# Performance work log

Measured on AMD Instinct MI355X. Metric: run time of the kernel, lower is better.

The kernel has to match this reference:

```python
import jax, jax.numpy as jnp
import numpy as np

B, S, D = 8, 1024, 1024      # batch, seq_len, inp_dim
H, HD = 8, 64                # head_num, head_dim
HID = H * HD                 # hidden_dim = 512
P = 2 * D                    # p_factor * inp_dim = 2048
K = 4                        # causal conv kernel size
EPS = 1e-6
CAP = 15.0                   # soft cap for i/f gates


def _layernorm(x, g, b):
    mu = jnp.mean(x, -1, keepdims=True)
    var = jnp.var(x, -1, keepdims=True)
    return (x - mu) * jax.lax.rsqrt(var + EPS) * g + b


def _soft_cap(v):
    return CAP * jnp.tanh(v / CAP)


def _causal_conv_feat(x, w, b):
    # Conv1d(1,1,K) applied over the FEATURE axis of each timestep (as in the
    # torch code: x_t.unsqueeze(1) -> (bs,1,P)), causal left pad of K-1.
    L = x.shape[-1]
    xp = jnp.pad(x, ((0, 0), (0, 0), (K - 1, 0)))
    out = b
    for m in range(K):
        out = out + w[m] * xp[..., m:m + L]
    return out


def _forward(x, ln_g, ln_b, mh_g, mh_b, W_up_l, b_up_l, W_up_r, b_up_r,
             W_down, b_down, conv_w, conv_b, W_skip, b_skip, W_i, b_i,
             W_f, b_f, W_o, b_o, W_q, b_q, W_k, b_k, W_v, b_v):
    Bs, Sl, _ = x.shape
    xn = _layernorm(x, ln_g, ln_b)
    x_t = xn @ W_up_l.T + b_up_l                      # (B,S,P)
    r_t = xn @ W_up_r.T + b_up_r                      # (B,S,HID)
    x_c = jax.nn.silu(_causal_conv_feat(x_t, conv_w, conv_b))
    x_skip = x_c @ W_skip.T + b_skip                  # (B,S,HID)
    q = (x_c @ W_q.T + b_q).reshape(Bs, Sl, H, HD)
    k = (x_c @ W_k.T + b_k).reshape(Bs, Sl, H, HD) / float(np.sqrt(HD))
    v = (x_t @ W_v.T + b_v).reshape(Bs, Sl, H, HD)
    i_pre = _soft_cap(x_c @ W_i.T + b_i)              # (B,S,H)
    f_pre = _soft_cap(x_c @ W_f.T + b_f)              # (B,S,H)
    o = jax.nn.sigmoid(x_t @ W_o.T + b_o)             # (B,S,HID)

    def step(carry, inp):
        c, n, m = carry
        qt, kt, vt, it, ft = inp
        m_t = jnp.maximum(ft + m, it)
        ie = jnp.exp(it - m_t)
        fe = jnp.exp(ft - m_t + m)
        c = fe[:, :, None, None] * c + ie[:, :, None, None] * jnp.einsum('bhd,bhe->bhde', vt, kt)
        n = fe[:, :, None] * n + ie[:, :, None] * kt
        num = jnp.einsum('bhde,bhe->bhd', c, qt)
        den = jnp.maximum(jnp.sum(n * qt, -1, keepdims=True), 1.0)
        return (c, n, m_t), num / den

    c0 = jnp.zeros((Bs, H, HD, HD), x.dtype)
    n0 = jnp.ones((Bs, H, HD), x.dtype)
    m0 = jnp.zeros((Bs, H), x.dtype)
    seq = tuple(jnp.moveaxis(a, 1, 0) for a in (q, k, v, i_pre, f_pre))
    _, hs = jax.lax.scan(step, (c0, n0, m0), seq)     # hs: (S,B,H,HD)
    h = o * jnp.moveaxis(hs, 0, 1).reshape(Bs, Sl, HID)
    hn = _layernorm(h.reshape(Bs, Sl, H, HD), mh_g, mh_b).reshape(Bs, Sl, HID)
    out = (hn + x_skip) * jax.nn.silu(r_t)
    return out @ W_down.T + b_down + x


def setup_inputs() -> dict:
    key = jax.random.key(0)
    ks = jax.random.split(key, 16)

    def w(kk, shape):
        return jax.random.normal(kk, shape, jnp.float32) / np.sqrt(shape[-1]).astype(np.float32)

    return {
        'x': jax.random.normal(ks[0], (B, S, D), jnp.float32),
        'ln_g': jnp.ones((D,), jnp.float32), 'ln_b': jnp.zeros((D,), jnp.float32),
        'mh_g': jnp.ones((H, HD), jnp.float32), 'mh_b': jnp.zeros((H, HD), jnp.float32),
        'W_up_l': w(ks[1], (P, D)), 'b_up_l': jnp.zeros((P,), jnp.float32),
        'W_up_r': w(ks[2], (HID, D)), 'b_up_r': jnp.zeros((HID,), jnp.float32),
        'W_down': w(ks[3], (D, HID)), 'b_down': jnp.zeros((D,), jnp.float32),
        'conv_w': jax.random.normal(ks[4], (K,), jnp.float32) * 0.3,
        'conv_b': jnp.zeros((), jnp.float32),
        'W_skip': w(ks[5], (HID, P)), 'b_skip': jnp.zeros((HID,), jnp.float32),
        'W_i': w(ks[6], (H, P)), 'b_i': jnp.zeros((H,), jnp.float32),
        'W_f': w(ks[7], (H, P)), 'b_f': jnp.zeros((H,), jnp.float32),
        'W_o': w(ks[8], (HID, P)), 'b_o': jnp.zeros((HID,), jnp.float32),
        'W_q': w(ks[9], (HID, P)), 'b_q': jnp.zeros((HID,), jnp.float32),
        'W_k': w(ks[10], (HID, P)), 'b_k': jnp.zeros((HID,), jnp.float32),
        'W_v': w(ks[11], (HID, P)), 'b_v': jnp.zeros((HID,), jnp.float32),
    }


def reference(x, ln_g, ln_b, mh_g, mh_b, W_up_l, b_up_l, W_up_r, b_up_r,
              W_down, b_down, conv_w, conv_b, W_skip, b_skip, W_i, b_i,
              W_f, b_f, W_o, b_o, W_q, b_q, W_k, b_k, W_v, b_v):
    return _forward(x, ln_g, ln_b, mh_g, mh_b, W_up_l, b_up_l, W_up_r, b_up_r,
                    W_down, b_down, conv_w, conv_b, W_skip, b_skip, W_i, b_i,
                    W_f, b_f, W_o, b_o, W_q, b_q, W_k, b_k, W_v, b_v)
```

## Files before the change

kernel.cpp:

```cpp
#include <hip/hip_runtime.h>
#include <hip/hip_bf16.h>
#include <math.h>

#define Bq 8
#define Sq 1024
#define Dq 1024
#define Hq 8
#define HDq 64
#define HIDq 512
#define Pq 2048
#define EPSq 1e-6f
#define CAPq 15.0f
#define NCq 16
#define CLq 64
#define ARENA_SH 4096
#define BUF_SH   (4 * ARENA_SH)
#define GEMM_SMEM_BYTES (2 * BUF_SH * 2)

typedef __attribute__((ext_vector_type(8))) short short8;
typedef __attribute__((ext_vector_type(4))) float f32x4v;
typedef __hip_bfloat16 bf16;

__device__ inline void split2(float v, bf16& h, bf16& l) {
  h = __float2bfloat16(v);
  l = __float2bfloat16(v - __bfloat162float(h));
}

__device__ inline float bfs2f(short s) {
  bf16 t = *(const bf16*)&s;
  return __bfloat162float(t);
}

__global__ __launch_bounds__(256) void cvtw_all(
    const float* __restrict__ s0, const float* __restrict__ s1,
    const float* __restrict__ s2, const float* __restrict__ s3,
    const float* __restrict__ s4, const float* __restrict__ s5,
    const float* __restrict__ s6, const float* __restrict__ s7,
    bf16* __restrict__ hi, bf16* __restrict__ lo)
{
  int u = blockIdx.x * 256 + threadIdx.x;
  const float* src; int segBase;
  if      (u <  524288) { src = s0; segBase = 0;       }
  else if (u <  655360) { src = s1; segBase = 524288;  }
  else if (u <  917504) { src = s2; segBase = 655360;  }
  else if (u < 1179648) { src = s3; segBase = 917504;  }
  else if (u < 1441792) { src = s4; segBase = 1179648; }
  else if (u < 1703936) { src = s5; segBase = 1441792; }
  else if (u < 1966080) { src = s6; segBase = 1703936; }
  else                  { src = s7; segBase = 1966080; }
  float4 v = ((const float4*)src)[u - segBase];
  size_t o = (size_t)u * 4;
  bf16 h, l;
  split2(v.x, h, l); hi[o+0] = h; lo[o+0] = l;
  split2(v.y, h, l); hi[o+1] = h; lo[o+1] = l;
  split2(v.z, h, l); hi[o+2] = h; lo[o+2] = l;
  split2(v.w, h, l); hi[o+3] = h; lo[o+3] = l;
}

__global__ __launch_bounds__(256) void ln_kernel(const float* __restrict__ x,
    const float* __restrict__ g, const float* __restrict__ b,
    bf16* __restrict__ yh, bf16* __restrict__ yl)
{
  int row = blockIdx.x;
  int tid = threadIdx.x;
  const float* xr = x + (size_t)row * Dq;
  float v[4]; float s = 0.f, s2 = 0.f;
  #pragma unroll
  for (int i = 0; i < 4; i++) { v[i] = xr[tid + 256*i]; s += v[i]; s2 += v[i]*v[i]; }
  #pragma unroll
  for (int mm = 32; mm > 0; mm >>= 1) { s += __shfl_xor(s, mm, 64); s2 += __shfl_xor(s2, mm, 64); }
  __shared__ float rs[4], rs2[4];
  int lane = tid & 63, wave = tid >> 6;
  if (lane == 0) { rs[wave] = s; rs2[wave] = s2; }
  __syncthreads();
  s  = rs[0] + rs[1] + rs[2] + rs[3];
  s2 = rs2[0] + rs2[1] + rs2[2] + rs2[3];
  float mu  = s * (1.f / Dq);
  float var = s2 * (1.f / Dq) - mu * mu;
  float r = rsqrtf(var + EPSq);
  #pragma unroll
  for (int i = 0; i < 4; i++) {
    int c = tid + 256*i;
    float y = (v[i] - mu) * r * g[c] + b[c];
    bf16 h, l; split2(y, h, l);
    yh[(size_t)row * Dq + c] = h;
    yl[(size_t)row * Dq + c] = l;
  }
}

__device__ __forceinline__ void stage_arena(short* ldsArena, const short* g,
                                            int Kd, int k0, int lane)
{
  int rsub = lane >> 2;
  int cs = (lane & 3) ^ ((lane >> 3) & 3);
  const short* gp = g + (size_t)rsub * Kd + k0 + cs * 8;
  short* lp = ldsArena;
  #pragma unroll
  for (int j = 0; j < 8; j++) {
    __builtin_amdgcn_global_load_lds(
        (const __attribute__((address_space(1))) void*)gp,
        (__attribute__((address_space(3))) void*)lp, 16, 0, 0);
    gp += (size_t)16 * Kd;
    lp += 512;
  }
}

__global__ __launch_bounds__(256) void gemm_x3(
    const bf16* __restrict__ Ahi, const bf16* __restrict__ Alo,
    const bf16* __restrict__ Whi, const bf16* __restrict__ Wlo,
    int Kd, int start1, int start2, const float* __restrict__ resid,
    const float* bias0, float* f0, bf16* h0, bf16* l0, int w0, float sc0, int a0,
    const float* bias1, float* f1, bf16* h1, bf16* l1, int w1, float sc1, int a1,
    const float* bias2, float* f2, bf16* h2, bf16* l2, int w2, float sc2, int a2)
{
  extern __shared__ short smem[];
  int tid = threadIdx.x;
  int lane = tid & 63, wave = tid >> 6;
  int wr = wave >> 1, wc = wave & 1;

  int gx = gridDim.x;
  int flat = blockIdx.y * gx + blockIdx.x;
  int nb = gx * gridDim.y;
  int chunk = nb >> 3;
  int nid = (flat & 7) * chunk + (flat >> 3);
  int col = nid % gx, row = nid / gx;
  int rowBase = row * 128;
  int colBase = col * 128;

  const short* Ahg = (const short*)Ahi + (size_t)rowBase * Kd;
  const short* Alg = (const short*)Alo + (size_t)rowBase * Kd;
  const short* Bhg = (const short*)Whi + (size_t)colBase * Kd;
  const short* Blg = (const short*)Wlo + (size_t)colBase * Kd;

  const short* src = (wave == 0) ? Ahg : (wave == 1) ? Alg
                   : (wave == 2) ? Bhg : Blg;
  short* arena0 = smem + wave * ARENA_SH;
  short* arena1 = smem + BUF_SH + wave * ARENA_SH;

  f32x4v acc[4][4];
  #pragma unroll
  for (int i = 0; i < 4; i++)
    #pragma unroll
    for (int j = 0; j < 4; j++) acc[i][j] = (f32x4v){0.f, 0.f, 0.f, 0.f};

  int fr = lane & 15;
  int cch = lane >> 4;
  int slotOff = ((cch ^ ((fr >> 1) & 3)) << 3);
  int nk = Kd >> 5;

  stage_arena(arena0, src, Kd, 0, lane);
  asm volatile("s_waitcnt vmcnt(0)" ::: "memory");
  __builtin_amdgcn_s_barrier();

  for (int t = 0; t < nk; ++t) {
    const short* Cb = smem + (t & 1) * BUF_SH;
    short* nxt = (t & 1) ? arena0 : arena1;
    if (t + 1 < nk) stage_arena(nxt, src, Kd, (t + 1) * 32, lane);

    short8 afh[4], afl[4], bfh[4], bfl[4];
    #pragma unroll
    for (int mi = 0; mi < 4; mi++) {
      int Ra = (wr * 64 + mi * 16 + fr) * 32;
      afh[mi] = *(const short8*)&Cb[0 * ARENA_SH + Ra + slotOff];
      afl[mi] = *(const short8*)&Cb[1 * ARENA_SH + Ra + slotOff];
    }
    #pragma unroll
    for (int ni = 0; ni < 4; ni++) {
      int Rb = (wc * 64 + ni * 16 + fr) * 32;
      bfh[ni] = *(const short8*)&Cb[2 * ARENA_SH + Rb + slotOff];
      bfl[ni] = *(const short8*)&Cb[3 * ARENA_SH + Rb + slotOff];
    }
    #pragma unroll
    for (int mi = 0; mi < 4; mi++)
      #pragma unroll
      for (int ni = 0; ni < 4; ni++)
        acc[mi][ni] = __builtin_amdgcn_mfma_f32_16x16x32_bf16(afh[mi], bfh[ni], acc[mi][ni], 0, 0, 0);
    #pragma unroll
    for (int mi = 0; mi < 4; mi++)
      #pragma unroll
      for (int ni = 0; ni < 4; ni++)
        acc[mi][ni] = __builtin_amdgcn_mfma_f32_16x16x32_bf16(afh[mi], bfl[ni], acc[mi][ni], 0, 0, 0);
    #pragma unroll
    for (int mi = 0; mi < 4; mi++)
      #pragma unroll
      for (int ni = 0; ni < 4; ni++)
        acc[mi][ni] = __builtin_amdgcn_mfma_f32_16x16x32_bf16(afl[mi], bfh[ni], acc[mi][ni], 0, 0, 0);

    asm volatile("s_waitcnt vmcnt(0)" ::: "memory");
    __builtin_amdgcn_s_barrier();
  }

  const float* bias; float* fOut; bf16* hOut; bf16* lOut; int segStart, segW; float sscale; int sact;
  if (colBase >= start2)      { bias=bias2; fOut=f2; hOut=h2; lOut=l2; segStart=start2; segW=w2; sscale=sc2; sact=a2; }
  else if (colBase >= start1) { bias=bias1; fOut=f1; hOut=h1; lOut=l1; segStart=start1; segW=w1; sscale=sc1; sact=a1; }
  else                        { bias=bias0; fOut=f0; hOut=h0; lOut=l0; segStart=0;      segW=w0; sscale=sc0; sact=a0; }

  int cr = (lane >> 4) * 4;
  int cc = lane & 15;
  #pragma unroll
  for (int mi = 0; mi < 4; mi++) {
    #pragma unroll
    for (int ni = 0; ni < 4; ni++) {
      int colO  = colBase + wc * 64 + ni * 16 + cc;
      int colL = colO - segStart;
      float bv = bias[colL];
      #pragma unroll
      for (int j = 0; j < 4; j++) {
        int rowO = rowBase + wr * 64 + mi * 16 + cr + j;
        float val = (acc[mi][ni][j] + bv) * sscale;
        if (sact) val = 1.f / (1.f + expf(-val));
        if (resid && segStart == 0) val += resid[(size_t)rowO * segW + colL];
        size_t oidx = (size_t)rowO * segW + colL;
        if (fOut) fOut[oidx] = val;
        if (hOut) {
          bf16 h, l; split2(val, h, l);
          hOut[oidx] = h; lOut[oidx] = l;
        }
      }
    }
  }
}

__global__ __launch_bounds__(256) void conv_kernel(const bf16* __restrict__ xth,
    const bf16* __restrict__ xtl, const float* __restrict__ cw,
    const float* __restrict__ cb, bf16* __restrict__ xch, bf16* __restrict__ xcl,
    int total8)
{
  int u = blockIdx.x * 256 + threadIdx.x;
  if (u >= total8) return;
  size_t idx = (size_t)u * 8;
  int p0 = (int)(idx & (Pq - 1));
  const short* hp = (const short*)xth + idx;
  const short* lp = (const short*)xtl + idx;
  short8 ch = *(const short8*)hp;
  short8 cl = *(const short8*)lp;
  float xv[11];
  #pragma unroll
  for (int j = 0; j < 8; j++) xv[3 + j] = bfs2f(ch[j]) + bfs2f(cl[j]);
  if (p0 > 0) {
    short8 ph = *(const short8*)(hp - 8);
    short8 pl = *(const short8*)(lp - 8);
    xv[0] = bfs2f(ph[5]) + bfs2f(pl[5]);
    xv[1] = bfs2f(ph[6]) + bfs2f(pl[6]);
    xv[2] = bfs2f(ph[7]) + bfs2f(pl[7]);
  } else {
    xv[0] = xv[1] = xv[2] = 0.f;
  }
  float w0 = cw[0], w1 = cw[1], w2 = cw[2], w3 = cw[3], bb = cb[0];
  short8 oh, ol;
  #pragma unroll
  for (int j = 0; j < 8; j++) {
    float acc = bb + w3 * xv[j + 3] + w2 * xv[j + 2] + w1 * xv[j + 1] + w0 * xv[j];
    float y = acc / (1.f + expf(-acc));
    bf16 h, l; split2(y, h, l);
    oh[j] = *(const short*)&h;
    ol[j] = *(const short*)&l;
  }
  *(short8*)((short*)xch + idx) = oh;
  *(short8*)((short*)xcl + idx) = ol;
}

__global__ __launch_bounds__(256) void ifk_kernel(const bf16* __restrict__ xch,
    const bf16* __restrict__ xcl,
    const float* __restrict__ Wi, const float* __restrict__ bi,
    const float* __restrict__ Wf, const float* __restrict__ bf_,
    float* __restrict__ ip, float* __restrict__ fp)
{
  int row = blockIdx.x;
  int lane = threadIdx.x & 63, wave = threadIdx.x >> 6;
  size_t rb = (size_t)row * Pq;
  const short* xh = (const short*)xch + rb;
  const short* xl = (const short*)xcl + rb;
  for (int oi = wave; oi < 16; oi += 4) {
    int hh = oi & 7;
    const float* Wrow = (oi < 8) ? (Wi + (size_t)hh * Pq) : (Wf + (size_t)hh * Pq);
    float s = 0.f;
    for (int j0 = lane * 8; j0 < Pq; j0 += 512) {
      short8 hv = *(const short8*)(xh + j0);
      short8 lv = *(const short8*)(xl + j0);
      float4 wa = *(const float4*)(Wrow + j0);
      float4 wb = *(const float4*)(Wrow + j0 + 4);
      s += (bfs2f(hv[0]) + bfs2f(lv[0])) * wa.x;
      s += (bfs2f(hv[1]) + bfs2f(lv[1])) * wa.y;
      s += (bfs2f(hv[2]) + bfs2f(lv[2])) * wa.z;
      s += (bfs2f(hv[3]) + bfs2f(lv[3])) * wa.w;
      s += (bfs2f(hv[4]) + bfs2f(lv[4])) * wb.x;
      s += (bfs2f(hv[5]) + bfs2f(lv[5])) * wb.y;
      s += (bfs2f(hv[6]) + bfs2f(lv[6])) * wb.z;
      s += (bfs2f(hv[7]) + bfs2f(lv[7])) * wb.w;
    }
    #pragma unroll
    for (int mm = 32; mm > 0; mm >>= 1) s += __shfl_xor(s, mm, 64);
    if (lane == 0) {
      float val = s + ((oi < 8) ? bi[hh] : bf_[hh]);
      val = CAPq * tanhf(val / CAPq);
      if (oi < 8) ip[(size_t)row * Hq + hh] = val;
      else        fp[(size_t)row * Hq + hh] = val;
    }
  }
}

__global__ __launch_bounds__(256) void chunkA_kernel(const float* __restrict__ k,
    const float* __restrict__ v, const float* __restrict__ ip,
    const float* __restrict__ fp, float* __restrict__ bg,
    float* __restrict__ FcMc, float* __restrict__ kvg, float* __restrict__ ksumg)
{
  int blk = blockIdx.x;
  int bh = blk >> 4, c = blk & 15;
  int b = bh >> 3, hh = bh & 7;
  int tid = threadIdx.x, lane = tid & 63, wave = tid >> 6;

  __shared__ float sK[64][64], sV[64][64], sW[64];

  size_t base = (size_t)b * Sq * 512 + (size_t)hh * 64 + (size_t)c * CLq * 512;
  int tr = tid >> 4, c4 = (tid & 15) * 4;
  #pragma unroll
  for (int p = 0; p < 4; p++) {
    int t = p * 16 + tr;
    *(float4*)&sK[t][c4] = *(const float4*)(k + base + (size_t)t * 512 + c4);
    *(float4*)&sV[t][c4] = *(const float4*)(v + base + (size_t)t * 512 + c4);
  }
  if (tid < 64) {
    size_t ifb = ((size_t)b * Sq + c * CLq + tid) * Hq + hh;
    float fv = fp[ifb], iv = ip[ifb];
    float cf = fv;
    #pragma unroll
    for (int off = 1; off < 64; off <<= 1) {
      float t2 = __shfl_up(cf, off, 64);
      if (lane >= off) cf += t2;
    }
    float bs = iv - cf;
    float mx = bs;
    #pragma unroll
    for (int off = 1; off < 64; off <<= 1) {
      float t2 = __shfl_up(mx, off, 64);
      if (lane >= off) mx = fmaxf(mx, t2);
    }
    float Mc = __shfl(mx, 63, 64);
    bg[(size_t)blk * 64 + tid] = bs;
    sW[tid] = expf(bs - Mc);
    if (tid == 63) { FcMc[blk*2] = cf; FcMc[blk*2+1] = Mc; }
  }
  __syncthreads();
  float acc[16];
  #pragma unroll
  for (int j = 0; j < 16; j++) acc[j] = 0.f;
  for (int s = 0; s < 64; s++) {
    float wv = sW[s] * sV[s][lane];
    #pragma unroll
    for (int j = 0; j < 16; j++) acc[j] += wv * sK[s][wave*16+j];
  }
  float* kvp = kvg + (size_t)blk * 4096 + lane * 64 + wave * 16;
  #pragma unroll
  for (int j = 0; j < 16; j++) kvp[j] = acc[j];
  if (tid < 64) {
    float a = 0.f;
    for (int s = 0; s < 64; s++) a += sW[s] * sK[s][tid];
    ksumg[(size_t)blk * 64 + tid] = a;
  }
}

__global__ __launch_bounds__(1024) void chunkB_kernel(const float* __restrict__ kvg,
    const float* __restrict__ ksumg, const float* __restrict__ FcMc,
    float* __restrict__ boundC, float* __restrict__ boundN, float* __restrict__ boundM)
{
  int bh = blockIdx.x;
  int tid = threadIdx.x;
  int r  = tid >> 4;
  int cq = (tid & 15) * 4;
  float4 C4 = {0.f, 0.f, 0.f, 0.f};
  float ne = 1.0f, m = 0.f;
  for (int c = 0; c < NCq; c++) {
    size_t blk = (size_t)bh * NCq + c;
    *(float4*)(boundC + blk * 4096 + r * 64 + cq) = C4;
    if ((tid & 15) == 0) boundN[blk * 64 + r] = ne;
    if (tid == 0)        boundM[blk] = m;
    float Fc = FcMc[blk * 2], Mc = FcMc[blk * 2 + 1];
    float mm = fmaxf(m, Mc);
    float a1 = expf(m - mm), a2 = expf(Mc - mm);
    float4 kv = *(const float4*)(kvg + blk * 4096 + r * 64 + cq);
    C4.x = a1 * C4.x + a2 * kv.x;
    C4.y = a1 * C4.y + a2 * kv.y;
    C4.z = a1 * C4.z + a2 * kv.z;
    C4.w = a1 * C4.w + a2 * kv.w;
    ne = a1 * ne + a2 * ksumg[blk * 64 + r];
    m = Fc + mm;
  }
}

__global__ __launch_bounds__(256) void chunkCE_kernel(const float* __restrict__ q,
    const float* __restrict__ k, const float* __restrict__ v,
    const float* __restrict__ bg, const float* __restrict__ boundC,
    const float* __restrict__ boundN, const float* __restrict__ boundM,
    const float* __restrict__ ov, const float* __restrict__ xs,
    const float* __restrict__ rt, const float* __restrict__ mg,
    const float* __restrict__ mb, bf16* __restrict__ pdh, bf16* __restrict__ pdl)
{
  int blk = blockIdx.x;
  int bh = blk >> 4, c = blk & 15;
  int b = bh >> 3, hh = bh & 7;
  int tid = threadIdx.x, lane = tid & 63, wave = tid >> 6;

  __shared__ float sQ[64][65], sKV[64][65], sS[64][65];
  __shared__ float sB[64], sMr[64], sNin[64];
  __shared__ float sLs[4][64], sLs2[4][64];

  size_t base = (size_t)b * Sq * 512 + (size_t)hh * 64 + (size_t)c * CLq * 512;
  int tr = tid >> 4, c4 = (tid & 15) * 4;
  #pragma unroll
  for (int p = 0; p < 4; p++) {
    int t = p * 16 + tr;
    float4 qv = *(const float4*)(q + base + (size_t)t * 512 + c4);
    float4 kv = *(const float4*)(k + base + (size_t)t * 512 + c4);
    sQ[t][c4+0] = qv.x; sQ[t][c4+1] = qv.y; sQ[t][c4+2] = qv.z; sQ[t][c4+3] = qv.w;
    sKV[t][c4+0] = kv.x; sKV[t][c4+1] = kv.y; sKV[t][c4+2] = kv.z; sKV[t][c4+3] = kv.w;
  }
  float m_in = boundM[blk];
  if (tid < 64) {
    float bs = bg[(size_t)blk * 64 + tid];
    float mx = bs;
    #pragma unroll
    for (int off = 1; off < 64; off <<= 1) {
      float t2 = __shfl_up(mx, off, 64);
      if (lane >= off) mx = fmaxf(mx, t2);
    }
    sB[tid]   = bs;
    sMr[tid]  = fmaxf(m_in, mx);
    sNin[tid] = boundN[(size_t)blk * 64 + tid];
  }
  __syncthreads();

  {
    int t = lane;
    float acc[16];
    #pragma unroll
    for (int j = 0; j < 16; j++) acc[j] = 0.f;
    for (int d = 0; d < 64; d++) {
      float qv = sQ[t][d];
      #pragma unroll
      for (int j = 0; j < 16; j++) acc[j] += qv * sKV[wave*16+j][d];
    }
    float Mr = sMr[t];
    #pragma unroll
    for (int j = 0; j < 16; j++) {
      int s = wave * 16 + j;
      float w = (s <= t) ? expf(sB[s] - Mr) : 0.f;
      sS[t][s] = w * acc[j];
    }
  }
  __syncthreads();
  #pragma unroll
  for (int p = 0; p < 4; p++) {
    int t = p * 16 + tr;
    float4 vv = *(const float4*)(v + base + (size_t)t * 512 + c4);
    sKV[t][c4+0] = vv.x; sKV[t][c4+1] = vv.y; sKV[t][c4+2] = vv.z; sKV[t][c4+3] = vv.w;
  }
  __syncthreads();

  {
    int t = lane;
    float Mr = sMr[t];
    float bfac = expf(m_in - Mr);
    float den = 0.f;
    for (int d = 0; d < 64; d++) den += sNin[d] * sQ[t][d];
    den *= bfac;
    float num[16];
    #pragma unroll
    for (int j = 0; j < 16; j++) num[j] = 0.f;
    const float* Crow = boundC + (size_t)blk * 4096;
    for (int e = 0; e < 64; e++) {
      float qv = sQ[t][e];
      #pragma unroll
      for (int j = 0; j < 16; j++)
        num[j] += Crow[(size_t)(wave*16+j) * 64 + e] * qv;
    }
    #pragma unroll
    for (int j = 0; j < 16; j++) num[j] *= bfac;
    for (int s = 0; s < 64; s++) {
      float ws = sS[t][s];
      den += ws;
      #pragma unroll
      for (int j = 0; j < 16; j++) num[j] += ws * sKV[s][wave*16+j];
    }
    den = fmaxf(den, 1.0f);

    size_t gidx = base + (size_t)t * 512 + (size_t)wave * 16;
    float hv[16];
    float s1 = 0.f, s2 = 0.f;
    #pragma unroll
    for (int j4 = 0; j4 < 4; j4++) {
      float4 og = *(const float4*)(ov + gidx + j4 * 4);
      float o0 = og.x * (num[j4*4+0] / den);
      float o1 = og.y * (num[j4*4+1] / den);
      float o2 = og.z * (num[j4*4+2] / den);
      float o3 = og.w * (num[j4*4+3] / den);
      hv[j4*4+0] = o0; hv[j4*4+1] = o1; hv[j4*4+2] = o2; hv[j4*4+3] = o3;
      s1 += o0 + o1 + o2 + o3;
      s2 += o0*o0 + o1*o1 + o2*o2 + o3*o3;
    }
    sLs[wave][t] = s1; sLs2[wave][t] = s2;
    __syncthreads();
    float S  = sLs[0][t] + sLs[1][t] + sLs[2][t] + sLs[3][t];
    float S2 = sLs2[0][t] + sLs2[1][t] + sLs2[2][t] + sLs2[3][t];
    float mu  = S * (1.f / 64.f);
    float var = S2 * (1.f / 64.f) - mu * mu;
    float rr = rsqrtf(var + EPSq);
    short8 ohv[2], olv[2];
    #pragma unroll
    for (int j4 = 0; j4 < 4; j4++) {
      float4 xsv = *(const float4*)(xs + gidx + j4 * 4);
      float4 rtv = *(const float4*)(rt + gidx + j4 * 4);
      #pragma unroll
      for (int e = 0; e < 4; e++) {
        int j = j4 * 4 + e;
        int d = wave * 16 + j;
        float hn = (hv[j] - mu) * rr * mg[hh * 64 + d] + mb[hh * 64 + d];
        float xsj = (e == 0) ? xsv.x : (e == 1) ? xsv.y : (e == 2) ? xsv.z : xsv.w;
        float rtj = (e == 0) ? rtv.x : (e == 1) ? rtv.y : (e == 2) ? rtv.z : rtv.w;
        float y = (hn + xsj) * (rtj / (1.f + expf(-rtj)));
        bf16 h, l; split2(y, h, l);
        ohv[j >> 3][j & 7] = *(const short*)&h;
        olv[j >> 3][j & 7] = *(const short*)&l;
      }
    }
    *(short8*)((short*)pdh + gidx) = ohv[0];
    *(short8*)((short*)pdh + gidx + 8) = ohv[1];
    *(short8*)((short*)pdl + gidx) = olv[0];
    *(short8*)((short*)pdl + gidx + 8) = olv[1];
  }
}

extern "C" void kernel_launch(void* const* d_in, const int* in_sizes, int n_in,
                              void* d_out, int out_size, void* d_ws, size_t ws_size,
                              hipStream_t stream)
{
  const float* x      = (const float*)d_in[0];
  const float* ln_g   = (const float*)d_in[1];
  const float* ln_b   = (const float*)d_in[2];
  const float* mh_g   = (const float*)d_in[3];
  const float* mh_b   = (const float*)d_in[4];
  const float* W_up_l = (const float*)d_in[5];
  const float* b_up_l = (const float*)d_in[6];
  const float* W_up_r = (const float*)d_in[7];
  const float* b_up_r = (const float*)d_in[8];
  const float* W_down = (const float*)d_in[9];
  const float* b_down = (const float*)d_in[10];
  const float* conv_w = (const float*)d_in[11];
  const float* conv_b = (const float*)d_in[12];
  const float* W_skip = (const float*)d_in[13];
  const float* b_skip = (const float*)d_in[14];
  const float* W_i    = (const float*)d_in[15];
  const float* b_i    = (const float*)d_in[16];
  const float* W_f    = (const float*)d_in[17];
  const float* b_f    = (const float*)d_in[18];
  const float* W_o    = (const float*)d_in[19];
  const float* b_o    = (const float*)d_in[20];
  const float* W_q    = (const float*)d_in[21];
  const float* b_q    = (const float*)d_in[22];
  const float* W_k    = (const float*)d_in[23];
  const float* b_k    = (const float*)d_in[24];
  const float* W_v    = (const float*)d_in[25];
  const float* b_v    = (const float*)d_in[26];
  float* out = (float*)d_out;

  const size_t MB = 1u << 20;
  if (ws_size < 193 * MB) return;

  char* base = (char*)d_ws;
  bf16* whi = (bf16*)base;
  bf16* wlo = (bf16*)(base + 16*MB);
  bf16* xnh = (bf16*)(base + 32*MB);
  bf16* xnl = (bf16*)(base + 48*MB);
  bf16* xth = (bf16*)(base + 64*MB);
  bf16* xtl = (bf16*)(base + 96*MB);
  bf16* xch = (bf16*)(base + 128*MB);
  bf16* xcl = (bf16*)(base + 160*MB);
  float* vb  = (float*)(base + 32*MB);
  float* ob  = (float*)(base + 48*MB);
  float* xs  = (float*)(base + 64*MB);
  float* qb  = (float*)(base + 80*MB);
  float* kb  = (float*)(base + 96*MB);
  bf16*  pdh = (bf16*)(base + 112*MB);
  bf16*  pdl = (bf16*)(base + 120*MB);
  float* kvg    = (float*)(base + 128*MB);
  float* boundC = (float*)(base + 144*MB);
  float* bg     = (float*)(base + 160*MB);
  float* ksumg  = (float*)(base + 160*MB + 256*1024);
  float* boundN = (float*)(base + 160*MB + 512*1024);
  float* FcMc   = (float*)(base + 160*MB + 768*1024);
  float* boundM = (float*)(base + 160*MB + 776*1024);
  float* ip  = (float*)(base + 192*MB);
  float* fpb = (float*)(base + 192*MB + 256*1024);
  float* rt  = out;

  const int Mrows = Bq * Sq;
  const int BIG = 1 << 30;

  cvtw_all<<<dim3(8192), dim3(256), 0, stream>>>(
      W_up_l, W_up_r, W_v, W_o, W_skip, W_q, W_k, W_down, whi, wlo);

  ln_kernel<<<dim3(Mrows), dim3(256), 0, stream>>>(x, ln_g, ln_b, xnh, xnl);

  gemm_x3<<<dim3(20, 64), dim3(256), GEMM_SMEM_BYTES, stream>>>(
      xnh, xnl, whi, wlo, 1024, 2048, BIG, nullptr,
      b_up_l, nullptr, xth, xtl, 2048, 1.f, 0,
      b_up_r, rt, nullptr, nullptr, 512, 1.f, 0,
      nullptr, nullptr, nullptr, nullptr, 1, 1.f, 0);

  gemm_x3<<<dim3(8, 64), dim3(256), GEMM_SMEM_BYTES, stream>>>(
      xth, xtl, whi + 2621440, wlo + 2621440, 2048, 512, BIG, nullptr,
      b_v, vb, nullptr, nullptr, 512, 1.f, 0,
      b_o, ob, nullptr, nullptr, 512, 1.f, 1,
      nullptr, nullptr, nullptr, nullptr, 1, 1.f, 0);

  int convTotal8 = Mrows * Pq / 8;
  conv_kernel<<<dim3(convTotal8 / 256), dim3(256), 0, stream>>>(
      xth, xtl, conv_w, conv_b, xch, xcl, convTotal8);

  gemm_x3<<<dim3(12, 64), dim3(256), GEMM_SMEM_BYTES, stream>>>(
      xch, xcl, whi + 4718592, wlo + 4718592, 2048, 512, 1024, nullptr,
      b_skip, xs, nullptr, nullptr, 512, 1.f, 0,
      b_q, qb, nullptr, nullptr, 512, 1.f, 0,
      b_k, kb, nullptr, nullptr, 512, 0.125f, 0);

  ifk_kernel<<<dim3(Mrows), dim3(256), 0, stream>>>(
      xch, xcl, W_i, b_i, W_f, b_f, ip, fpb);

  chunkA_kernel<<<dim3(Bq * Hq * NCq), dim3(256), 0, stream>>>(
      kb, vb, ip, fpb, bg, FcMc, kvg, ksumg);
  chunkB_kernel<<<dim3(Bq * Hq), dim3(1024), 0, stream>>>(
      kvg, ksumg, FcMc, boundC, boundN, boundM);
  chunkCE_kernel<<<dim3(Bq * Hq * NCq), dim3(256), 0, stream>>>(
      qb, kb, vb, bg, boundC, boundN, boundM, ob, xs, rt, mh_g, mh_b, pdh, pdl);

  gemm_x3<<<dim3(8, 64), dim3(256), GEMM_SMEM_BYTES, stream>>>(
      pdh, pdl, whi + 7864320, wlo + 7864320, 512, BIG, BIG, x,
      b_down, out, nullptr, nullptr, 1024, 1.f, 0,
      nullptr, nullptr, nullptr, nullptr, 1, 1.f, 0,
      nullptr, nullptr, nullptr, nullptr, 1, 1.f, 0);
}
```

Measured before the change: 833.8 us.

## Load A-low fragments directly from global and shrink GEMM LDS to three arenas

```diff
diff --git a/kernel.cpp b/kernel.cpp
--- a/kernel.cpp
+++ b/kernel.cpp
@@ -14,8 +14,8 @@
 #define NCq 16
 #define CLq 64
 #define ARENA_SH 4096
-#define BUF_SH   (4 * ARENA_SH)
-#define GEMM_SMEM_BYTES (2 * BUF_SH * 2)
+#define BUF3_SH  (3 * ARENA_SH)
+#define GEMM_SMEM_BYTES (2 * BUF3_SH * 2)
 
 typedef __attribute__((ext_vector_type(8))) short short8;
 typedef __attribute__((ext_vector_type(4))) float f32x4v;
@@ -88,24 +88,25 @@
   }
 }
 
-__device__ __forceinline__ void stage_arena(short* ldsArena, const short* g,
-                                            int Kd, int k0, int lane)
+__device__ __forceinline__ void stage3(short* buf, const short* Ahg,
+    const short* Bhg, const short* Blg, int Kd, int k0, int lane, int wave)
 {
   int rsub = lane >> 2;
   int cs = (lane & 3) ^ ((lane >> 3) & 3);
-  const short* gp = g + (size_t)rsub * Kd + k0 + cs * 8;
-  short* lp = ldsArena;
-  #pragma unroll
-  for (int j = 0; j < 8; j++) {
+  #pragma unroll
+  for (int j = 0; j < 6; j++) {
+    int g = wave * 6 + j;
+    int a = g >> 3, sIn = g & 7;
+    const short* srcb = (a == 0) ? Ahg : (a == 1) ? Bhg : Blg;
+    const short* gp = srcb + (size_t)(sIn * 16 + rsub) * Kd + k0 + cs * 8;
+    short* lp = buf + a * ARENA_SH + sIn * 16 * 32;
     __builtin_amdgcn_global_load_lds(
         (const __attribute__((address_space(1))) void*)gp,
         (__attribute__((address_space(3))) void*)lp, 16, 0, 0);
-    gp += (size_t)16 * Kd;
-    lp += 512;
-  }
-}
-
-__global__ __launch_bounds__(256) void gemm_x3(
+  }
+}
+
+__global__ __launch_bounds__(256, 3) void gemm_x3(
     const bf16* __restrict__ Ahi, const bf16* __restrict__ Alo,
     const bf16* __restrict__ Whi, const bf16* __restrict__ Wlo,
     int Kd, int start1, int start2, const float* __restrict__ resid,
@@ -128,15 +129,9 @@
   int colBase = col * 128;
 
   const short* Ahg = (const short*)Ahi + (size_t)rowBase * Kd;
-  const short* Alg = (const short*)Alo + (size_t)rowBase * Kd;
   const short* Bhg = (const short*)Whi + (size_t)colBase * Kd;
   const short* Blg = (const short*)Wlo + (size_t)colBase * Kd;
 
-  const short* src = (wave == 0) ? Ahg : (wave == 1) ? Alg
-                   : (wave == 2) ? Bhg : Blg;
-  short* arena0 = smem + wave * ARENA_SH;
-  short* arena1 = smem + BUF_SH + wave * ARENA_SH;
-
   f32x4v acc[4][4];
   #pragma unroll
   for (int i = 0; i < 4; i++)
@@ -145,30 +140,40 @@
 
   int fr = lane & 15;
   int cch = lane >> 4;
+  int fk = cch * 8;
   int slotOff = ((cch ^ ((fr >> 1) & 3)) << 3);
   int nk = Kd >> 5;
 
-  stage_arena(arena0, src, Kd, 0, lane);
+  const short* AlgF = (const short*)Alo
+      + (size_t)(rowBase + wr * 64 + fr) * Kd + fk;
+
+  stage3(smem, Ahg, Bhg, Blg, Kd, 0, lane, wave);
   asm volatile("s_waitcnt vmcnt(0)" ::: "memory");
   __builtin_amdgcn_s_barrier();
 
   for (int t = 0; t < nk; ++t) {
-    const short* Cb = smem + (t & 1) * BUF_SH;
-    short* nxt = (t & 1) ? arena0 : arena1;
-    if (t + 1 < nk) stage_arena(nxt, src, Kd, (t + 1) * 32, lane);
-
-    short8 afh[4], afl[4], bfh[4], bfl[4];
+    const short* Cb = smem + (t & 1) * BUF3_SH;
+    short* nxt = smem + ((t + 1) & 1) * BUF3_SH;
+
+    short8 aflg[4];
+    #pragma unroll
+    for (int mi = 0; mi < 4; mi++)
+      aflg[mi] = *(const short8*)(AlgF + (size_t)mi * 16 * Kd + t * 32);
+    __builtin_amdgcn_sched_barrier(0);
+
+    if (t + 1 < nk) stage3(nxt, Ahg, Bhg, Blg, Kd, (t + 1) * 32, lane, wave);
+
+    short8 afh[4], bfh[4], bfl[4];
     #pragma unroll
     for (int mi = 0; mi < 4; mi++) {
       int Ra = (wr * 64 + mi * 16 + fr) * 32;
       afh[mi] = *(const short8*)&Cb[0 * ARENA_SH + Ra + slotOff];
-      afl[mi] = *(const short8*)&Cb[1 * ARENA_SH + Ra + slotOff];
     }
     #pragma unroll
     for (int ni = 0; ni < 4; ni++) {
       int Rb = (wc * 64 + ni * 16 + fr) * 32;
-      bfh[ni] = *(const short8*)&Cb[2 * ARENA_SH + Rb + slotOff];
-      bfl[ni] = *(const short8*)&Cb[3 * ARENA_SH + Rb + slotOff];
+      bfh[ni] = *(const short8*)&Cb[1 * ARENA_SH + Rb + slotOff];
+      bfl[ni] = *(const short8*)&Cb[2 * ARENA_SH + Rb + slotOff];
     }
     #pragma unroll
     for (int mi = 0; mi < 4; mi++)
@@ -184,7 +189,7 @@
     for (int mi = 0; mi < 4; mi++)
       #pragma unroll
       for (int ni = 0; ni < 4; ni++)
-        acc[mi][ni] = __builtin_amdgcn_mfma_f32_16x16x32_bf16(afl[mi], bfh[ni], acc[mi][ni], 0, 0, 0);
+        acc[mi][ni] = __builtin_amdgcn_mfma_f32_16x16x32_bf16(aflg[mi], bfh[ni], acc[mi][ni], 0, 0, 0);
 
     asm volatile("s_waitcnt vmcnt(0)" ::: "memory");
     __builtin_amdgcn_s_barrier();
```

Result: slower. 864.3 us (+3.7%).
